# Performance work log

Measured on AMD Instinct MI355X. Metric: run time of the kernel, lower is better.

The kernel has to match this reference:

```python
import jax, jax.numpy as jnp
import numpy as np

L, N_ATOMS, N_PROBES, E, H = 3, 20000, 100000, 400000, 128
CUTOFF, STEP, EDGE_SIZE = 4.0, 0.25, 16
LOG2 = float(np.log(2.0))

def ssp(x):
    # ShiftedSoftplus: softplus(x) - log(2)
    return jax.nn.softplus(x) - LOG2

def mlp(x, W1, b1, W2, b2):
    return ssp(x @ W1 + b1) @ W2 + b2

def setup_inputs() -> dict:
    key = jax.random.key(0)
    ks = iter(jax.random.split(key, 32))
    def nrm(shape, s=0.05):
        return jax.random.normal(next(ks), shape, dtype=jnp.float32) * s
    inp = {
        'atom_rep': nrm((L, N_ATOMS, H), 1.0),
        'dist': jax.random.uniform(next(ks), (E, 1), dtype=jnp.float32) * CUTOFF,
    }
    pshapes = {
        'msg_We1': (L, EDGE_SIZE, H), 'msg_be1': (L, H),
        'msg_We2': (L, H, H), 'msg_be2': (L, H),
        'msg_Wn1': (L, 2 * H, H), 'msg_bn1': (L, H),
        'msg_Wn2': (L, H, H), 'msg_bn2': (L, H),
        'gate_W1': (L, H, H), 'gate_b1': (L, H),
        'gate_W2': (L, H, H), 'gate_b2': (L, H),
        'trans_W1': (L, H, H), 'trans_b1': (L, H),
        'trans_W2': (L, H, H), 'trans_b2': (L, H),
        'readout_W1': (H, H), 'readout_b1': (H,),
        'readout_W2': (H, 1), 'readout_b2': (1,),
    }
    for name, shp in pshapes.items():
        inp[name] = nrm(shp)
    senders = jax.random.randint(next(ks), (E, 1), 0, N_ATOMS)
    receivers = jax.random.randint(next(ks), (E, 1), 0, N_PROBES)
    inp['probe_edges'] = jnp.concatenate([senders, receivers], axis=1).astype(jnp.int32)
    return inp

def reference(atom_rep, dist, msg_We1, msg_be1, msg_We2, msg_be2, msg_Wn1, msg_bn1, msg_Wn2, msg_bn2, gate_W1, gate_b1, gate_W2, gate_b2, trans_W1, trans_b1, trans_W2, trans_b2, readout_W1, readout_b1, readout_W2, readout_b2, probe_edges):
    # gaussian_expansion of edge distances: [E, EDGE_SIZE]
    mu = jnp.arange(0.0, CUTOFF, STEP, dtype=jnp.float32)
    edge_state = jnp.exp(-((dist - mu) ** 2) / (2.0 * STEP * STEP))
    # SchnetMessageFunction soft cutoff on raw distance: [E, 1]
    soft_cut = 1.0 - jax.nn.sigmoid(5.0 * (dist - (CUTOFF - 1.5)))
    snd = probe_edges[:, 0]  # atom senders
    rcv = probe_edges[:, 1]  # probe receivers
    probe_state0 = jnp.zeros((N_PROBES, H), dtype=jnp.float32)

    def step(probe_state, layer):
        (nodes_l, We1, be1, We2, be2, Wn1, bn1, Wn2, bn2,
         gW1, gb1, gW2, gb2, tW1, tb1, tW2, tb2) = layer
        # edge filter gates [E, H]
        gates_msg = mlp(edge_state, We1, be1, We2, be2) * soft_cut
        # include_receiver=True with receiver_nodes=probe_state: concat sender atom / receiver probe
        nodes = jnp.concatenate([nodes_l[snd], probe_state[rcv]], axis=1)  # [E, 2H]
        messages = mlp(nodes, Wn1, bn1, Wn2, bn2) * gates_msg  # [E, H]
        msgsum = jax.ops.segment_sum(messages, rcv, num_segments=N_PROBES)  # [P, H]
        g = jax.nn.sigmoid(mlp(probe_state, gW1, gb1, gW2, gb2))
        new_state = probe_state * g + (1.0 - g) * mlp(msgsum, tW1, tb1, tW2, tb2)
        return new_state, None

    xs = (atom_rep, msg_We1, msg_be1, msg_We2, msg_be2, msg_Wn1, msg_bn1,
          msg_Wn2, msg_bn2, gate_W1, gate_b1, gate_W2, gate_b2,
          trans_W1, trans_b1, trans_W2, trans_b2)
    probe_state, _ = jax.lax.scan(step, probe_state0, xs)
    out = mlp(probe_state, readout_W1, readout_b1, readout_W2, readout_b2)[:, 0]  # [P]
    return out
```

## Files before the change

### kernel.cpp

```cpp
#include <hip/hip_runtime.h>

#define NLAYER 3
#define NATOM 20000
#define NPROBE 100000
#define NEDGE 400000
#define HD 128
#define NBIN 2048
#define CUTOFFF 4.0f
#define PLANE 16384
#define MT 64
#define NT 512
#define NSBLK ((NPROBE + 255) / 256)

typedef unsigned int u32;
typedef unsigned short u16;
typedef __attribute__((ext_vector_type(8))) short bf16x8;
typedef __attribute__((ext_vector_type(4))) float f32x4;

__device__ __forceinline__ float sspf(float x) {
    float e = __builtin_amdgcn_exp2f(fminf(x, 80.f) * 1.44269504088896341f);
    return 0.69314718055994531f * (__builtin_amdgcn_logf(1.f + e) - 1.f);
}
__device__ __forceinline__ float sigf(float x) {
    return 1.f / (1.f + __builtin_amdgcn_exp2f(-x * 1.44269504088896341f));
}
__device__ __forceinline__ void atomic_add_f(float* p, float v) {
    __hip_atomic_fetch_add(p, v, __ATOMIC_RELAXED, __HIP_MEMORY_SCOPE_AGENT);
}
__device__ __forceinline__ u32 atomic_add_u(u32* p, u32 v) {
    return __hip_atomic_fetch_add(p, v, __ATOMIC_RELAXED, __HIP_MEMORY_SCOPE_AGENT);
}
__device__ __forceinline__ u32 f2u(float f) { union { float f; u32 u; } x; x.f = f; return x.u; }
__device__ __forceinline__ float u2f(u32 u) { union { float f; u32 u; } x; x.u = u; return x.f; }
__device__ __forceinline__ u16 bf16rn(float f) {
    u32 u = f2u(f);
    u32 r = u + 0x7fffu + ((u >> 16) & 1u);
    return (u16)(r >> 16);
}
__device__ __forceinline__ u32 bf16pair(float x, float y) {
    u32 ux = f2u(x);
    u32 hx = (ux + 0x7fffu + ((ux >> 16) & 1u)) >> 16;
    u32 uy = f2u(y);
    u32 hy = (uy + 0x7fffu + ((uy >> 16) & 1u)) & 0xffff0000u;
    return hx | hy;
}
__device__ __forceinline__ void split_pair(float x, float y, u32& hi, u32& lo) {
    u32 ux = f2u(x);
    u32 hx = (ux + 0x7fffu + ((ux >> 16) & 1u)) & 0xffff0000u;
    float lxf = x - u2f(hx);
    u32 uy = f2u(y);
    u32 hy = (uy + 0x7fffu + ((uy >> 16) & 1u)) & 0xffff0000u;
    float lyf = y - u2f(hy);
    hi = (hx >> 16) | hy;
    lo = (f2u(lxf) >> 16) | (f2u(lyf) & 0xffff0000u);
}

__device__ __forceinline__ void bar_lds() {
    asm volatile("s_waitcnt lgkmcnt(0)" ::: "memory");
    __builtin_amdgcn_s_barrier();
}

__device__ __forceinline__ int bswz(int b, int nb) {
    int q = nb >> 3, r = nb & 7;
    int x = b & 7, o = b >> 3;
    return (x < r ? x * (q + 1) : r * (q + 1) + (x - r) * q) + o;
}

__device__ __forceinline__ void load_bfrags(const u16* __restrict__ Wb, int lane, int wid,
                                            bf16x8 Bh[4], bf16x8 Bl[4]) {
    const bf16x8* Bhp = (const bf16x8*)Wb;
    const bf16x8* Blp = (const bf16x8*)(Wb + PLANE);
#pragma unroll
    for (int c = 0; c < 4; ++c) {
        Bh[c] = Bhp[(size_t)(c * 8 + wid) * 64 + lane];
        Bl[c] = Blp[(size_t)(c * 8 + wid) * 64 + lane];
    }
}

__device__ __forceinline__ void mma_slice_pre(const u16* __restrict__ ldsH,
                                              const u16* __restrict__ ldsL,
                                              int lane, const bf16x8 Bh[4], const bf16x8 Bl[4],
                                              f32x4 acc[4]) {
    int l15 = lane & 15, kq = lane >> 4;
#pragma unroll
    for (int m = 0; m < 4; ++m) {
        int row = m * 16 + l15;
        int s = row & 7;
        const u16* hp = ldsH + row * 128;
        const u16* lp = ldsL + row * 128;
#pragma unroll
        for (int c = 0; c < 4; ++c) {
            int off = ((c * 4 + kq) ^ s) << 3;
            bf16x8 Ah = *(const bf16x8*)(hp + off);
            bf16x8 Al = *(const bf16x8*)(lp + off);
            acc[m] = __builtin_amdgcn_mfma_f32_16x16x32_bf16(Ah, Bh[c], acc[m], 0, 0, 0);
            acc[m] = __builtin_amdgcn_mfma_f32_16x16x32_bf16(Al, Bh[c], acc[m], 0, 0, 0);
            acc[m] = __builtin_amdgcn_mfma_f32_16x16x32_bf16(Ah, Bl[c], acc[m], 0, 0, 0);
        }
    }
}

__device__ __forceinline__ void mma_slice(const u16* __restrict__ ldsH,
                                          const u16* __restrict__ ldsL,
                                          int lane, int wid,
                                          const u16* __restrict__ Wb,
                                          f32x4 acc[4]) {
    bf16x8 Bh[4], Bl[4];
    load_bfrags(Wb, lane, wid, Bh, Bl);
    mma_slice_pre(ldsH, ldsL, lane, Bh, Bl, acc);
}

__device__ __forceinline__ void mma_slice_a1(const u16* __restrict__ ldsA,
                                             int lane, const bf16x8 Bh[4], const bf16x8 Bl[4],
                                             f32x4 acc[4]) {
    int l15 = lane & 15, kq = lane >> 4;
#pragma unroll
    for (int m = 0; m < 4; ++m) {
        int row = m * 16 + l15;
        int s = row & 7;
        const u16* ap = ldsA + row * 128;
#pragma unroll
        for (int c = 0; c < 4; ++c) {
            int off = ((c * 4 + kq) ^ s) << 3;
            bf16x8 Ah = *(const bf16x8*)(ap + off);
            acc[m] = __builtin_amdgcn_mfma_f32_16x16x32_bf16(Ah, Bh[c], acc[m], 0, 0, 0);
            acc[m] = __builtin_amdgcn_mfma_f32_16x16x32_bf16(Ah, Bl[c], acc[m], 0, 0, 0);
        }
    }
}

__device__ __forceinline__ void mma_w_a1(const u16* __restrict__ ldsA,
                                         int lane, int wid, const u16* __restrict__ Wb,
                                         f32x4 acc[4]) {
    bf16x8 Bh[4], Bl[4];
    load_bfrags(Wb, lane, wid, Bh, Bl);
    mma_slice_a1(ldsA, lane, Bh, Bl, acc);
}

__device__ __forceinline__ void pack_store(const float* v, int row, int q,
                                           u16* ldsH, u16* ldsL) {
    int s = row & 7;
#pragma unroll
    for (int h = 0; h < 2; ++h) {
        u32 hv[4], lv[4];
#pragma unroll
        for (int k = 0; k < 4; ++k)
            split_pair(v[8 * h + 2 * k], v[8 * h + 2 * k + 1], hv[k], lv[k]);
        int gc = q * 2 + h;
        int off = row * 128 + ((gc ^ s) << 3);
        *(uint4*)(ldsH + off) = make_uint4(hv[0], hv[1], hv[2], hv[3]);
        *(uint4*)(ldsL + off) = make_uint4(lv[0], lv[1], lv[2], lv[3]);
    }
}

__device__ __forceinline__ void pack_plane(const float* v, int row, int q, u16* ldsA) {
    int s = row & 7;
#pragma unroll
    for (int h = 0; h < 2; ++h) {
        u32 w0 = bf16pair(v[8 * h + 0], v[8 * h + 1]);
        u32 w1 = bf16pair(v[8 * h + 2], v[8 * h + 3]);
        u32 w2 = bf16pair(v[8 * h + 4], v[8 * h + 5]);
        u32 w3 = bf16pair(v[8 * h + 6], v[8 * h + 7]);
        int gc = q * 2 + h;
        *(uint4*)(ldsA + row * 128 + ((gc ^ s) << 3)) = make_uint4(w0, w1, w2, w3);
    }
}

__device__ __forceinline__ void gather_rows(const float* __restrict__ A, int M,
                                            int m0, int t, float* v) {
    int r = t >> 3, q = t & 7;
    int row = m0 + r;
    bool ok = row < M;
    const float4* src = (const float4*)(A + (size_t)row * HD + q * 16);
#pragma unroll
    for (int j = 0; j < 4; ++j) {
        float4 x = ok ? src[j] : make_float4(0.f, 0.f, 0.f, 0.f);
        v[4 * j] = x.x; v[4 * j + 1] = x.y; v[4 * j + 2] = x.z; v[4 * j + 3] = x.w;
    }
}
__device__ __forceinline__ void zero_rows(float* A, int M, int m0, int t) {
    int r = t >> 3, q = t & 7;
    int row = m0 + r;
    if (row < M) {
        float4* dst = (float4*)(A + (size_t)row * HD + q * 16);
        float4 z = make_float4(0.f, 0.f, 0.f, 0.f);
#pragma unroll
        for (int j = 0; j < 4; ++j) dst[j] = z;
    }
}
__device__ __forceinline__ void stage_split(const float* __restrict__ A, int M,
                                            int m0, int t, u16* ldsH, u16* ldsL) {
    float v[16];
    gather_rows(A, M, m0, t, v);
    pack_store(v, t >> 3, t & 7, ldsH, ldsL);
}
__device__ __forceinline__ void stage_plane(const float* __restrict__ A, int M,
                                            int m0, int t, u16* ldsA) {
    float v[16];
    gather_rows(A, M, m0, t, v);
    pack_plane(v, t >> 3, t & 7, ldsA);
}

__device__ __forceinline__ void h_store(u16* ldsH, u16* ldsL, int wid, int lane,
                                        const f32x4 acc[4], const float* __restrict__ bias) {
    int l15 = lane & 15, lq = lane >> 4;
    int col = wid * 16 + l15;
    float bb = bias[col];
    int gc = col >> 3, wg = col & 7;
#pragma unroll
    for (int m = 0; m < 4; ++m) {
#pragma unroll
        for (int r = 0; r < 4; ++r) {
            int row = m * 16 + lq * 4 + r;
            float h = sspf(acc[m][r] + bb);
            u32 u = f2u(h);
            u32 hh = (u + 0x7fffu + ((u >> 16) & 1u)) & 0xffff0000u;
            float lf = h - u2f(hh);
            int off = row * 128 + ((gc ^ (row & 7)) << 3) + wg;
            ldsH[off] = (u16)(hh >> 16);
            ldsL[off] = (u16)(f2u(lf) >> 16);
        }
    }
}
__device__ __forceinline__ void h_plane(u16* ldsA, int wid, int lane,
                                        const f32x4 acc[4], const float* __restrict__ bias) {
    int l15 = lane & 15, lq = lane >> 4;
    int col = wid * 16 + l15;
    float bb = bias[col];
    int gc = col >> 3, wg = col & 7;
#pragma unroll
    for (int m = 0; m < 4; ++m) {
#pragma unroll
        for (int r = 0; r < 4; ++r) {
            int row = m * 16 + lq * 4 + r;
            int off = row * 128 + ((gc ^ (row & 7)) << 3) + wg;
            ldsA[off] = bf16rn(sspf(acc[m][r] + bb));
        }
    }
}
__device__ __forceinline__ void v_store(u16* ldsH, u16* ldsL, int wid, int lane,
                                        int m, int r, float val) {
    int l15 = lane & 15, lq = lane >> 4;
    int col = wid * 16 + l15;
    int gc = col >> 3, wg = col & 7;
    int row = m * 16 + lq * 4 + r;
    u32 u = f2u(val);
    u32 hh = (u + 0x7fffu + ((u >> 16) & 1u)) & 0xffff0000u;
    float lf = val - u2f(hh);
    int off = row * 128 + ((gc ^ (row & 7)) << 3) + wg;
    ldsH[off] = (u16)(hh >> 16);
    ldsL[off] = (u16)(f2u(lf) >> 16);
}
__device__ __forceinline__ void v_plane(u16* ldsA, int wid, int lane,
                                        int m, int r, float val) {
    int l15 = lane & 15, lq = lane >> 4;
    int col = wid * 16 + l15;
    int gc = col >> 3, wg = col & 7;
    int row = m * 16 + lq * 4 + r;
    ldsA[row * 128 + ((gc ^ (row & 7)) << 3) + wg] = bf16rn(val);
}

__global__ void convert_w_k(const float* __restrict__ Wn1, const float* __restrict__ Wn2,
                            const float* __restrict__ gW1, const float* __restrict__ gW2,
                            const float* __restrict__ tW1, const float* __restrict__ tW2,
                            const float* __restrict__ rW1, u16* __restrict__ Wb) {
    int m = blockIdx.x;
    const float* src;
    if (m < 6)       src = Wn1 + (size_t)(m >> 1) * (2 * HD * HD) + (size_t)(m & 1) * (HD * HD);
    else if (m < 9)  src = Wn2 + (size_t)(m - 6) * HD * HD;
    else if (m < 12) src = gW1 + (size_t)(m - 9) * HD * HD;
    else if (m < 15) src = gW2 + (size_t)(m - 12) * HD * HD;
    else if (m < 18) src = tW1 + (size_t)(m - 15) * HD * HD;
    else if (m < 21) src = tW2 + (size_t)(m - 18) * HD * HD;
    else             src = rW1;
    int t = threadIdx.x;
    int lane = t & 63, nn = t >> 6;
    u16* dh = Wb + (size_t)m * (2 * PLANE);
    u16* dl = dh + PLANE;
    for (int c = 0; c < 4; ++c) {
        for (int hh = 0; hh < 2; ++hh) {
            int n = nn + hh * 4;
            int col = n * 16 + (lane & 15);
            int k0 = c * 32 + (lane >> 4) * 8;
            u32 hv[4], lv[4];
#pragma unroll
            for (int jj = 0; jj < 4; ++jj) {
                float wA = src[(size_t)(k0 + 2 * jj) * HD + col];
                float wB = src[(size_t)(k0 + 2 * jj + 1) * HD + col];
                u16 ha = bf16rn(wA), hb = bf16rn(wB);
                u16 la = bf16rn(wA - u2f((u32)ha << 16));
                u16 lb = bf16rn(wB - u2f((u32)hb << 16));
                hv[jj] = (u32)ha | ((u32)hb << 16);
                lv[jj] = (u32)la | ((u32)lb << 16);
            }
            size_t off = ((size_t)(c * 8 + n) * 64 + lane) * 8;
            *(uint4*)(dh + off) = make_uint4(hv[0], hv[1], hv[2], hv[3]);
            *(uint4*)(dl + off) = make_uint4(lv[0], lv[1], lv[2], lv[3]);
        }
    }
}

__global__ void gate_table_k(const float* __restrict__ We1, const float* __restrict__ be1,
                             const float* __restrict__ We2, const float* __restrict__ be2,
                             float2* __restrict__ gt2) {
    int row = blockIdx.x;
    int l = row / (NBIN + 1);
    int i = row % (NBIN + 1);
    int j = threadIdx.x;
    float d = (CUTOFFF / NBIN) * (float)i;
    __shared__ float h1[HD];
    const float* w1 = We1 + (size_t)l * 16 * HD;
    float acc = be1[l * HD + j];
#pragma unroll
    for (int k = 0; k < 16; ++k) {
        float dd = d - 0.25f * (float)k;
        float es = __builtin_amdgcn_exp2f(-dd * dd * 8.0f * 1.44269504088896341f);
        acc = fmaf(es, w1[k * HD + j], acc);
    }
    h1[j] = sspf(acc);
    __syncthreads();
    const float* w2 = We2 + (size_t)l * HD * HD;
    float acc2 = be2[l * HD + j];
    for (int k = 0; k < HD; ++k) acc2 = fmaf(h1[k], w2[k * HD + j], acc2);
    float sc = 1.f - sigf(5.f * (d - (CUTOFFF - 1.5f)));
    float val = acc2 * sc;
    float2* base = gt2 + (size_t)l * NBIN * HD;
    if (i < NBIN) base[(size_t)i * HD + j].x = val;
    if (i > 0)    base[(size_t)(i - 1) * HD + j].y = val;
}

__global__ void gate0_k(const float* __restrict__ gW2, const float* __restrict__ gb1,
                        const float* __restrict__ gb2, float* __restrict__ g0v) {
    int j = threadIdx.x;
    __shared__ float h[HD];
    h[j] = sspf(gb1[j]);
    __syncthreads();
    float acc = gb2[j];
    for (int k = 0; k < HD; ++k) acc = fmaf(h[k], gW2[k * HD + j], acc);
    g0v[j] = sigf(acc);
}

__global__ __launch_bounds__(256) void hist_k(const int* __restrict__ pe, u32* __restrict__ cnt) {
    int e = blockIdx.x * 256 + threadIdx.x;
    if (e < NEDGE) atomic_add_u(&cnt[pe[2 * e + 1]], 1u);
}

__global__ __launch_bounds__(256) void bsum_k(const u32* __restrict__ cnt, u32* __restrict__ bsum) {
    int i = blockIdx.x * 256 + threadIdx.x;
    int v = (i < NPROBE) ? (int)cnt[i] : 0;
#pragma unroll
    for (int d = 1; d < 64; d <<= 1) v += __shfl_xor(v, d);
    __shared__ int wsum[4];
    if ((threadIdx.x & 63) == 0) wsum[threadIdx.x >> 6] = v;
    __syncthreads();
    if (threadIdx.x == 0) bsum[blockIdx.x] = (u32)(wsum[0] + wsum[1] + wsum[2] + wsum[3]);
}

__global__ __launch_bounds__(512) void bscan_k(u32* __restrict__ bsum) {
    __shared__ u32 s[512];
    int t = threadIdx.x;
    u32 v = (t < NSBLK) ? bsum[t] : 0u;
    s[t] = v;
    __syncthreads();
    for (int d = 1; d < 512; d <<= 1) {
        u32 x = (t >= d) ? s[t - d] : 0u;
        __syncthreads();
        s[t] += x;
        __syncthreads();
    }
    if (t < NSBLK) bsum[t] = s[t] - v;
}

__global__ __launch_bounds__(256) void cur_k(const u32* __restrict__ cnt,
                                             const u32* __restrict__ bsum, u32* __restrict__ cur) {
    __shared__ u32 s[256];
    int b = blockIdx.x, t = threadIdx.x;
    int i = b * 256 + t;
    u32 v = (i < NPROBE) ? cnt[i] : 0u;
    s[t] = v;
    __syncthreads();
    for (int d = 1; d < 256; d <<= 1) {
        u32 x = (t >= d) ? s[t - d] : 0u;
        __syncthreads();
        s[t] += x;
        __syncthreads();
    }
    if (i < NPROBE) cur[i] = bsum[b] + s[t] - v;
}

__global__ __launch_bounds__(256) void scatter_k(const int* __restrict__ pe,
                                                 u32* __restrict__ cur, u32* __restrict__ eord) {
    int e = blockIdx.x * 256 + threadIdx.x;
    if (e < NEDGE) {
        u32 pos = atomic_add_u(&cur[pe[2 * e + 1]], 1u);
        eord[pos] = (u32)e;
    }
}

#define ABLK 313
__global__ __launch_bounds__(NT, 4) void gemm_atoms_k(const float* __restrict__ atom_rep,
                                                      const u16* __restrict__ Wb,
                                                      const float* __restrict__ bn1,
                                                      u16* __restrict__ Xab) {
    __shared__ u16 ldsH[MT * 128];
    __shared__ u16 ldsL[MT * 128];
    int l = blockIdx.x / ABLK;
    int mb = blockIdx.x % ABLK;
    const float* A = atom_rep + (size_t)l * NATOM * HD;
    const u16* W = Wb + (size_t)(2 * l) * 2 * PLANE;
    u16* outp = Xab + (size_t)l * NATOM * HD;
    int m0 = mb * MT, t = threadIdx.x;
    stage_split(A, NATOM, m0, t, ldsH, ldsL);
    bar_lds();
    int lane = t & 63, wid = t >> 6;
    int l15 = lane & 15, lq = lane >> 4;
    int col = wid * 16 + l15;
    f32x4 acc[4] = {};
    mma_slice(ldsH, ldsL, lane, wid, W, acc);
    float bv = bn1[l * HD + col];
#pragma unroll
    for (int m = 0; m < 4; ++m) {
#pragma unroll
        for (int r = 0; r < 4; ++r) {
            int row = m0 + m * 16 + lq * 4 + r;
            if (row < NATOM) outp[(size_t)row * HD + col] = bf16rn(acc[m][r] + bv);
        }
    }
}

__device__ __forceinline__ int rho(int r) {
    return ((r >> 2) & 3) * 16 + ((r >> 4) << 2) + (r & 3);
}

__device__ __forceinline__ void gather_edge(
        int e0, int t, const u16* __restrict__ Xab, const u16* __restrict__ Xp,
        const int* __restrict__ pe, const u32* __restrict__ eord,
        const float* __restrict__ dist,
        u32* mix_s, float* fr_s, float* sum) {
    int r = t >> 3, q = t & 7;
    int e = (int)eord[e0 + r];
    int snd = pe[2 * e], rcv = pe[2 * e + 1];
    if (q == 0) {
        float x = dist[e] * ((float)NBIN / CUTOFFF);
        int i = (int)x;
        i = i < (NBIN - 1) ? i : (NBIN - 1);
        fr_s[r] = x - (float)i;
        mix_s[r] = ((u32)rcv << 11) | (u32)i;
    }
    const uint4* xa4 = (const uint4*)(Xab + (size_t)snd * HD + q * 16);
    u32 aw[8];
    *(uint4*)aw = xa4[0];
    *(uint4*)(aw + 4) = xa4[1];
    u32 pw[8];
    if (Xp) {
        const uint4* xp4 = (const uint4*)(Xp + (size_t)rcv * HD + q * 16);
        *(uint4*)pw = xp4[0];
        *(uint4*)(pw + 4) = xp4[1];
    }
#pragma unroll
    for (int w = 0; w < 8; ++w) {
        float ae = u2f(aw[w] << 16), ao = u2f(aw[w] & 0xffff0000u);
        if (Xp) {
            ae += u2f(pw[w] << 16);
            ao += u2f(pw[w] & 0xffff0000u);
        }
        sum[2 * w] = ae;
        sum[2 * w + 1] = ao;
    }
}

__device__ __forceinline__ void edge_out(const f32x4 acc[4], const u32* mix_s,
        const float* fr_s, const float2* __restrict__ gt2,
        float bb, int col, int lq, float* __restrict__ msgsum) {
    float carry = 0.f;
    int rcc = -1;
#pragma unroll
    for (int m = 3; m >= 0; --m) {
        int ebase = lq * 16 + m * 4;
        float vals[4];
        int rc[4];
#pragma unroll
        for (int r = 0; r < 4; ++r) {
            u32 mx = mix_s[ebase + r];
            rc[r] = (int)(mx >> 11);
            float2 g2 = gt2[(size_t)(mx & 2047u) * HD + col];
            vals[r] = (acc[m][r] + bb) * fmaf(g2.y - g2.x, fr_s[ebase + r], g2.x);
        }
        if (rcc == rc[3]) vals[3] += carry;
        else if (rcc >= 0) atomic_add_f(msgsum + (size_t)rcc * HD + col, carry);
#pragma unroll
        for (int r = 3; r >= 1; --r) {
            if (rc[r] == rc[r - 1]) vals[r - 1] += vals[r];
            else atomic_add_f(msgsum + (size_t)rc[r] * HD + col, vals[r]);
        }
        carry = vals[0];
        rcc = rc[0];
    }
    atomic_add_f(msgsum + (size_t)rcc * HD + col, carry);
}

__global__ __launch_bounds__(NT, 4) void edge_msg_k(
        const u16* __restrict__ Xab, const u16* __restrict__ Xp,
        const u16* __restrict__ W2b, const float* __restrict__ bn2,
        const float2* __restrict__ gt2, const float* __restrict__ dist,
        const int* __restrict__ pe, const u32* __restrict__ eord,
        float* __restrict__ msgsum) {
    __shared__ u16 ldsA[MT * 128];
    __shared__ u32 mix_s[MT];
    __shared__ float fr_s[MT];
    int t = threadIdx.x;
    int lane = t & 63, wid = t >> 6;
    int l15 = lane & 15, lq = lane >> 4;
    int col = wid * 16 + l15;
    const int nb = NEDGE / MT;
    int e0 = bswz(blockIdx.x, nb) * MT;

    bf16x8 Bh[4], Bl[4];
    load_bfrags(W2b, lane, wid, Bh, Bl);
    float bb = bn2[col];

    float s0[16];
    gather_edge(e0, t, Xab, Xp, pe, eord, dist, mix_s, fr_s, s0);
    {
        float h[16];
#pragma unroll
        for (int k = 0; k < 16; ++k) h[k] = sspf(s0[k]);
        pack_plane(h, rho(t >> 3), t & 7, ldsA);
    }
    bar_lds();

    f32x4 acc[4] = {};
    mma_slice_a1(ldsA, lane, Bh, Bl, acc);
    edge_out(acc, mix_s, fr_s, gt2, bb, col, lq, msgsum);
}

__global__ __launch_bounds__(NT, 4) void probe_update_k(
        const float* ps, const float* msgsum, float* msgzero,
        const u16* __restrict__ gW1b, const float* __restrict__ gb1,
        const u16* __restrict__ gW2b, const float* __restrict__ gb2,
        const u16* __restrict__ tW1b, const float* __restrict__ tb1,
        const u16* __restrict__ tW2b, const float* __restrict__ tb2,
        const u16* __restrict__ W3b,
        const u16* __restrict__ rW1b, const float* __restrict__ rb1,
        const float* __restrict__ rW2, const float* __restrict__ rb2,
        const float* __restrict__ g0v,
        float* psout, u16* __restrict__ xpout, float* __restrict__ outp) {
    __shared__ u16 ldsH[MT * 128];
    __shared__ u16 ldsL[MT * 128];
    __shared__ float parts[MT][9];
    int m0 = blockIdx.x * MT, t = threadIdx.x;
    int lane = t & 63, wid = t >> 6;
    int l15 = lane & 15, lq = lane >> 4;
    int col = wid * 16 + l15;

    f32x4 g[4] = {};
    f32x4 tv[4] = {};

    float sm[16];
    gather_rows(msgsum, NPROBE, m0, t, sm);

    if (!g0v) {
        stage_plane(ps, NPROBE, m0, t, ldsH);
        bar_lds();
        mma_w_a1(ldsH, lane, wid, gW1b, g);
        bar_lds();
        h_plane(ldsH, wid, lane, g, gb1);
        bar_lds();
#pragma unroll
        for (int m = 0; m < 4; ++m) g[m] = (f32x4){0.f, 0.f, 0.f, 0.f};
        mma_w_a1(ldsH, lane, wid, gW2b, g);
        float gb2v = gb2[col];
#pragma unroll
        for (int m = 0; m < 4; ++m)
#pragma unroll
            for (int r = 0; r < 4; ++r) g[m][r] = sigf(g[m][r] + gb2v);
        bar_lds();
    } else {
        float gv = g0v[col];
#pragma unroll
        for (int m = 0; m < 4; ++m)
#pragma unroll
            for (int r = 0; r < 4; ++r) g[m][r] = gv;
    }

    pack_store(sm, t >> 3, t & 7, ldsH, ldsL);
    if (msgzero) zero_rows(msgzero, NPROBE, m0, t);
    bar_lds();
    mma_slice(ldsH, ldsL, lane, wid, tW1b, tv);
    bar_lds();
    h_store(ldsH, ldsL, wid, lane, tv, tb1);
    bar_lds();
#pragma unroll
    for (int m = 0; m < 4; ++m) tv[m] = (f32x4){0.f, 0.f, 0.f, 0.f};
    mma_slice(ldsH, ldsL, lane, wid, tW2b, tv);

    bool isW3 = (W3b != nullptr);
    bool isRd = (rW1b != nullptr);
    if (isW3 || isRd) bar_lds();

    float tb2v = tb2[col];
#pragma unroll
    for (int m = 0; m < 4; ++m) {
#pragma unroll
        for (int r = 0; r < 4; ++r) {
            int row = m0 + m * 16 + lq * 4 + r;
            float val = 0.f;
            if (row < NPROBE) {
                size_t idx = (size_t)row * HD + col;
                float tval = tv[m][r] + tb2v;
                float pv = g0v ? 0.f : ps[idx];
                val = fmaf(pv - tval, g[m][r], tval);
                if (!isRd) psout[idx] = val;
            }
            if (isW3) v_plane(ldsH, wid, lane, m, r, val);
            else if (isRd) v_store(ldsH, ldsL, wid, lane, m, r, val);
        }
    }
    if (!(isW3 || isRd)) return;
    bar_lds();

    if (isW3) {
        f32x4 a[4] = {};
        mma_w_a1(ldsH, lane, wid, W3b, a);
#pragma unroll
        for (int m = 0; m < 4; ++m)
#pragma unroll
            for (int r = 0; r < 4; ++r) {
                int row = m0 + m * 16 + lq * 4 + r;
                if (row < NPROBE) xpout[(size_t)row * HD + col] = bf16rn(a[m][r]);
            }
    } else {
        f32x4 a[4] = {};
        mma_slice(ldsH, ldsL, lane, wid, rW1b, a);
        float rb1v = rb1[col], w2v = rW2[col];
#pragma unroll
        for (int m = 0; m < 4; ++m)
#pragma unroll
            for (int r = 0; r < 4; ++r) {
                float p = sspf(a[m][r] + rb1v) * w2v;
                p += __shfl_xor(p, 1, 16);
                p += __shfl_xor(p, 2, 16);
                p += __shfl_xor(p, 4, 16);
                p += __shfl_xor(p, 8, 16);
                if (l15 == 0) parts[m * 16 + lq * 4 + r][wid] = p;
            }
        bar_lds();
        if (t < MT) {
            int row = m0 + t;
            if (row < NPROBE) {
                float s = rb2[0];
#pragma unroll
                for (int w = 0; w < 8; ++w) s += parts[t][w];
                outp[row] = s;
            }
        }
    }
}

extern "C" void kernel_launch(void* const* d_in, const int* in_sizes, int n_in,
                              void* d_out, int out_size, void* d_ws, size_t ws_size,
                              hipStream_t stream) {
    const float* atom_rep = (const float*)d_in[0];
    const float* dist     = (const float*)d_in[1];
    const float* We1 = (const float*)d_in[2];
    const float* be1 = (const float*)d_in[3];
    const float* We2 = (const float*)d_in[4];
    const float* be2 = (const float*)d_in[5];
    const float* Wn1 = (const float*)d_in[6];
    const float* bn1 = (const float*)d_in[7];
    const float* Wn2 = (const float*)d_in[8];
    const float* bn2 = (const float*)d_in[9];
    const float* gW1 = (const float*)d_in[10];
    const float* gb1 = (const float*)d_in[11];
    const float* gW2 = (const float*)d_in[12];
    const float* gb2 = (const float*)d_in[13];
    const float* tW1 = (const float*)d_in[14];
    const float* tb1 = (const float*)d_in[15];
    const float* tW2 = (const float*)d_in[16];
    const float* tb2 = (const float*)d_in[17];
    const float* rW1 = (const float*)d_in[18];
    const float* rb1 = (const float*)d_in[19];
    const float* rW2 = (const float*)d_in[20];
    const float* rb2 = (const float*)d_in[21];
    const int*   pe  = (const int*)d_in[22];
    float* out = (float*)d_out;

    float* ws = (float*)d_ws;
    float* ps     = ws;
    float* msgsum = ps + 12800000u;
    float2* gt2   = (float2*)(msgsum + 12800000u);
    float* g0v    = (float*)(gt2 + (size_t)NLAYER * NBIN * HD);
    u16*   Wb     = (u16*)(g0v + 128);
    u16*   Xp16   = Wb + 22 * 2 * PLANE;
    u16*   Xab    = Xp16 + 12800000u;
    u32*   cnt    = (u32*)(Xab + 7680000u);
    u32*   bsum   = cnt + NPROBE;
    u32*   cur    = bsum + 512;
    u32*   eord   = cur + NPROBE;

    const int PBLK = (NPROBE + MT - 1) / MT;
    const int EBLK = NEDGE / MT;
    const int TBLK = (NEDGE + 255) / 256;

    hipMemsetAsync(cnt, 0, (size_t)NPROBE * 4, stream);
    hipMemsetAsync(msgsum, 0, 12800000ull * 4, stream);
    convert_w_k<<<22, 256, 0, stream>>>(Wn1, Wn2, gW1, gW2, tW1, tW2, rW1, Wb);
    gate_table_k<<<NLAYER * (NBIN + 1), HD, 0, stream>>>(We1, be1, We2, be2, gt2);
    gate0_k<<<1, HD, 0, stream>>>(gW2, gb1, gb2, g0v);
    hist_k<<<TBLK, 256, 0, stream>>>(pe, cnt);
    bsum_k<<<NSBLK, 256, 0, stream>>>(cnt, bsum);
    bscan_k<<<1, 512, 0, stream>>>(bsum);
    cur_k<<<NSBLK, 256, 0, stream>>>(cnt, bsum, cur);
    scatter_k<<<TBLK, 256, 0, stream>>>(pe, cur, eord);
    gemm_atoms_k<<<NLAYER * ABLK, NT, 0, stream>>>(atom_rep, Wb, bn1, Xab);

    for (int l = 0; l < NLAYER; ++l) {
        edge_msg_k<<<EBLK, NT, 0, stream>>>(Xab + (size_t)l * NATOM * HD,
                                            (l == 0) ? nullptr : Xp16,
                                            Wb + (size_t)(6 + l) * 2 * PLANE,
                                            bn2 + l * HD,
                                            gt2 + (size_t)l * NBIN * HD,
                                            dist, pe, eord, msgsum);
        const u16* W3  = (l < NLAYER - 1) ? Wb + (size_t)(2 * (l + 1) + 1) * 2 * PLANE : nullptr;
        const u16* RW1 = (l == NLAYER - 1) ? Wb + (size_t)21 * 2 * PLANE : nullptr;
        float* mz = (l < NLAYER - 1) ? msgsum : nullptr;
        probe_update_k<<<PBLK, NT, 0, stream>>>(ps, msgsum, mz,
                                                Wb + (size_t)(9 + l) * 2 * PLANE, gb1 + l * HD,
                                                Wb + (size_t)(12 + l) * 2 * PLANE, gb2 + l * HD,
                                                Wb + (size_t)(15 + l) * 2 * PLANE, tb1 + l * HD,
                                                Wb + (size_t)(18 + l) * 2 * PLANE, tb2 + l * HD,
                                                W3, RW1, rb1, rW2, rb2,
                                                (l == 0) ? g0v : nullptr,
                                                ps, Xp16, out);
    }
}
```

Before: 606.2 us.

## Fuse edge message and probe update into one per-probe-block kernel

Edge messages are now computed inside the probe-update kernel. Each probe block walks its contiguous receiver-sorted edge range (row starts come from the scan) and accumulates messages into a shared-memory tile instead of issuing global atomics into a full msgsum buffer. This removes the separate edge kernel, the large msgsum buffer with its memset and per-layer zeroing, and the global read-back of that buffer. In exchange, blocks loop over a variable number of edges, which can cause load imbalance, and the heavier shared-memory use lowers launch-bounds occupancy from 4 to 2.

```diff
diff --git a/kernel.cpp b/kernel.cpp
--- a/kernel.cpp
+++ b/kernel.cpp
@@ -10,6 +10,7 @@
 #define PLANE 16384
 #define MT 64
 #define NT 512
+#define PBLK ((NPROBE + MT - 1) / MT)
 #define NSBLK ((NPROBE + 255) / 256)
 
 typedef unsigned int u32;
@@ -23,9 +24,6 @@
 }
 __device__ __forceinline__ float sigf(float x) {
     return 1.f / (1.f + __builtin_amdgcn_exp2f(-x * 1.44269504088896341f));
-}
-__device__ __forceinline__ void atomic_add_f(float* p, float v) {
-    __hip_atomic_fetch_add(p, v, __ATOMIC_RELAXED, __HIP_MEMORY_SCOPE_AGENT);
 }
 __device__ __forceinline__ u32 atomic_add_u(u32* p, u32 v) {
     return __hip_atomic_fetch_add(p, v, __ATOMIC_RELAXED, __HIP_MEMORY_SCOPE_AGENT);
@@ -99,11 +97,9 @@
         }
     }
 }
-
 __device__ __forceinline__ void mma_slice(const u16* __restrict__ ldsH,
                                           const u16* __restrict__ ldsL,
-                                          int lane, int wid,
-                                          const u16* __restrict__ Wb,
+                                          int lane, int wid, const u16* __restrict__ Wb,
                                           f32x4 acc[4]) {
     bf16x8 Bh[4], Bl[4];
     load_bfrags(Wb, lane, wid, Bh, Bl);
@@ -128,7 +124,6 @@
         }
     }
 }
-
 __device__ __forceinline__ void mma_w_a1(const u16* __restrict__ ldsA,
                                          int lane, int wid, const u16* __restrict__ Wb,
                                          f32x4 acc[4]) {
@@ -152,7 +147,6 @@
         *(uint4*)(ldsL + off) = make_uint4(lv[0], lv[1], lv[2], lv[3]);
     }
 }
-
 __device__ __forceinline__ void pack_plane(const float* v, int row, int q, u16* ldsA) {
     int s = row & 7;
 #pragma unroll
@@ -165,7 +159,6 @@
         *(uint4*)(ldsA + row * 128 + ((gc ^ s) << 3)) = make_uint4(w0, w1, w2, w3);
     }
 }
-
 __device__ __forceinline__ void gather_rows(const float* __restrict__ A, int M,
                                             int m0, int t, float* v) {
     int r = t >> 3, q = t & 7;
@@ -178,27 +171,11 @@
         v[4 * j] = x.x; v[4 * j + 1] = x.y; v[4 * j + 2] = x.z; v[4 * j + 3] = x.w;
     }
 }
-__device__ __forceinline__ void zero_rows(float* A, int M, int m0, int t) {
-    int r = t >> 3, q = t & 7;
-    int row = m0 + r;
-    if (row < M) {
-        float4* dst = (float4*)(A + (size_t)row * HD + q * 16);
-        float4 z = make_float4(0.f, 0.f, 0.f, 0.f);
-#pragma unroll
-        for (int j = 0; j < 4; ++j) dst[j] = z;
-    }
-}
 __device__ __forceinline__ void stage_split(const float* __restrict__ A, int M,
                                             int m0, int t, u16* ldsH, u16* ldsL) {
     float v[16];
     gather_rows(A, M, m0, t, v);
     pack_store(v, t >> 3, t & 7, ldsH, ldsL);
-}
-__device__ __forceinline__ void stage_plane(const float* __restrict__ A, int M,
-                                            int m0, int t, u16* ldsA) {
-    float v[16];
-    gather_rows(A, M, m0, t, v);
-    pack_plane(v, t >> 3, t & 7, ldsA);
 }
 
 __device__ __forceinline__ void h_store(u16* ldsH, u16* ldsL, int wid, int lane,
@@ -344,7 +321,6 @@
     int e = blockIdx.x * 256 + threadIdx.x;
     if (e < NEDGE) atomic_add_u(&cnt[pe[2 * e + 1]], 1u);
 }
-
 __global__ __launch_bounds__(256) void bsum_k(const u32* __restrict__ cnt, u32* __restrict__ bsum) {
     int i = blockIdx.x * 256 + threadIdx.x;
     int v = (i < NPROBE) ? (int)cnt[i] : 0;
@@ -355,7 +331,6 @@
     __syncthreads();
     if (threadIdx.x == 0) bsum[blockIdx.x] = (u32)(wsum[0] + wsum[1] + wsum[2] + wsum[3]);
 }
-
 __global__ __launch_bounds__(512) void bscan_k(u32* __restrict__ bsum) {
     __shared__ u32 s[512];
     int t = threadIdx.x;
@@ -370,9 +345,9 @@
     }
     if (t < NSBLK) bsum[t] = s[t] - v;
 }
-
 __global__ __launch_bounds__(256) void cur_k(const u32* __restrict__ cnt,
-                                             const u32* __restrict__ bsum, u32* __restrict__ cur) {
+                                             const u32* __restrict__ bsum,
+                                             u32* __restrict__ cur, u32* __restrict__ rs) {
     __shared__ u32 s[256];
     int b = blockIdx.x, t = threadIdx.x;
     int i = b * 256 + t;
@@ -385,9 +360,15 @@
         s[t] += x;
         __syncthreads();
     }
-    if (i < NPROBE) cur[i] = bsum[b] + s[t] - v;
-}
-
+    if (i < NPROBE) {
+        u32 v0 = bsum[b] + s[t] - v;
+        cur[i] = v0;
+        rs[i] = v0;
+    }
+}
+__global__ void rstail_k(u32* __restrict__ rs) {
+    rs[NPROBE + threadIdx.x] = NEDGE;
+}
 __global__ __launch_bounds__(256) void scatter_k(const int* __restrict__ pe,
                                                  u32* __restrict__ cur, u32* __restrict__ eord) {
     int e = blockIdx.x * 256 + threadIdx.x;
@@ -432,46 +413,9 @@
     return ((r >> 2) & 3) * 16 + ((r >> 4) << 2) + (r & 3);
 }
 
-__device__ __forceinline__ void gather_edge(
-        int e0, int t, const u16* __restrict__ Xab, const u16* __restrict__ Xp,
-        const int* __restrict__ pe, const u32* __restrict__ eord,
-        const float* __restrict__ dist,
-        u32* mix_s, float* fr_s, float* sum) {
-    int r = t >> 3, q = t & 7;
-    int e = (int)eord[e0 + r];
-    int snd = pe[2 * e], rcv = pe[2 * e + 1];
-    if (q == 0) {
-        float x = dist[e] * ((float)NBIN / CUTOFFF);
-        int i = (int)x;
-        i = i < (NBIN - 1) ? i : (NBIN - 1);
-        fr_s[r] = x - (float)i;
-        mix_s[r] = ((u32)rcv << 11) | (u32)i;
-    }
-    const uint4* xa4 = (const uint4*)(Xab + (size_t)snd * HD + q * 16);
-    u32 aw[8];
-    *(uint4*)aw = xa4[0];
-    *(uint4*)(aw + 4) = xa4[1];
-    u32 pw[8];
-    if (Xp) {
-        const uint4* xp4 = (const uint4*)(Xp + (size_t)rcv * HD + q * 16);
-        *(uint4*)pw = xp4[0];
-        *(uint4*)(pw + 4) = xp4[1];
-    }
-#pragma unroll
-    for (int w = 0; w < 8; ++w) {
-        float ae = u2f(aw[w] << 16), ao = u2f(aw[w] & 0xffff0000u);
-        if (Xp) {
-            ae += u2f(pw[w] << 16);
-            ao += u2f(pw[w] & 0xffff0000u);
-        }
-        sum[2 * w] = ae;
-        sum[2 * w + 1] = ao;
-    }
-}
-
-__device__ __forceinline__ void edge_out(const f32x4 acc[4], const u32* mix_s,
+__device__ __forceinline__ void edge_out_lds(const f32x4 acc[4], const u32* mix_s,
         const float* fr_s, const float2* __restrict__ gt2,
-        float bb, int col, int lq, float* __restrict__ msgsum) {
+        float bb, int col, int lq, float* __restrict__ msg) {
     float carry = 0.f;
     int rcc = -1;
 #pragma unroll
@@ -482,60 +426,37 @@
 #pragma unroll
         for (int r = 0; r < 4; ++r) {
             u32 mx = mix_s[ebase + r];
-            rc[r] = (int)(mx >> 11);
-            float2 g2 = gt2[(size_t)(mx & 2047u) * HD + col];
-            vals[r] = (acc[m][r] + bb) * fmaf(g2.y - g2.x, fr_s[ebase + r], g2.x);
-        }
-        if (rcc == rc[3]) vals[3] += carry;
-        else if (rcc >= 0) atomic_add_f(msgsum + (size_t)rcc * HD + col, carry);
+            if (mx == 0xFFFFFFFFu) {
+                rc[r] = -2;
+                vals[r] = 0.f;
+            } else {
+                rc[r] = (int)(mx >> 11);
+                float2 g2 = gt2[(size_t)(mx & 2047u) * HD + col];
+                vals[r] = (acc[m][r] + bb) * fmaf(g2.y - g2.x, fr_s[ebase + r], g2.x);
+            }
+        }
+        if (rcc >= 0) {
+            if (rcc == rc[3]) vals[3] += carry;
+            else atomicAdd(&msg[rcc * HD + col], carry);
+        }
 #pragma unroll
         for (int r = 3; r >= 1; --r) {
             if (rc[r] == rc[r - 1]) vals[r - 1] += vals[r];
-            else atomic_add_f(msgsum + (size_t)rc[r] * HD + col, vals[r]);
+            else if (rc[r] >= 0) atomicAdd(&msg[rc[r] * HD + col], vals[r]);
         }
         carry = vals[0];
         rcc = rc[0];
     }
-    atomic_add_f(msgsum + (size_t)rcc * HD + col, carry);
-}
-
-__global__ __launch_bounds__(NT, 4) void edge_msg_k(
+    if (rcc >= 0) atomicAdd(&msg[rcc * HD + col], carry);
+}
+
+__global__ __launch_bounds__(NT, 2) void fused_layer_k(
         const u16* __restrict__ Xab, const u16* __restrict__ Xp,
         const u16* __restrict__ W2b, const float* __restrict__ bn2,
         const float2* __restrict__ gt2, const float* __restrict__ dist,
         const int* __restrict__ pe, const u32* __restrict__ eord,
-        float* __restrict__ msgsum) {
-    __shared__ u16 ldsA[MT * 128];
-    __shared__ u32 mix_s[MT];
-    __shared__ float fr_s[MT];
-    int t = threadIdx.x;
-    int lane = t & 63, wid = t >> 6;
-    int l15 = lane & 15, lq = lane >> 4;
-    int col = wid * 16 + l15;
-    const int nb = NEDGE / MT;
-    int e0 = bswz(blockIdx.x, nb) * MT;
-
-    bf16x8 Bh[4], Bl[4];
-    load_bfrags(W2b, lane, wid, Bh, Bl);
-    float bb = bn2[col];
-
-    float s0[16];
-    gather_edge(e0, t, Xab, Xp, pe, eord, dist, mix_s, fr_s, s0);
-    {
-        float h[16];
-#pragma unroll
-        for (int k = 0; k < 16; ++k) h[k] = sspf(s0[k]);
-        pack_plane(h, rho(t >> 3), t & 7, ldsA);
-    }
-    bar_lds();
-
-    f32x4 acc[4] = {};
-    mma_slice_a1(ldsA, lane, Bh, Bl, acc);
-    edge_out(acc, mix_s, fr_s, gt2, bb, col, lq, msgsum);
-}
-
-__global__ __launch_bounds__(NT, 4) void probe_update_k(
-        const float* ps, const float* msgsum, float* msgzero,
+        const u32* __restrict__ rs,
+        const float* ps,
         const u16* __restrict__ gW1b, const float* __restrict__ gb1,
         const u16* __restrict__ gW2b, const float* __restrict__ gb2,
         const u16* __restrict__ tW1b, const float* __restrict__ tb1,
@@ -545,36 +466,125 @@
         const float* __restrict__ rW2, const float* __restrict__ rb2,
         const float* __restrict__ g0v,
         float* psout, u16* __restrict__ xpout, float* __restrict__ outp) {
-    __shared__ u16 ldsH[MT * 128];
-    __shared__ u16 ldsL[MT * 128];
+    __shared__ float msg[MT * HD];
+    __shared__ u16 ldsA[MT * 128];
+    __shared__ u32 mix_s[MT];
+    __shared__ float fr_s[MT];
     __shared__ float parts[MT][9];
-    int m0 = blockIdx.x * MT, t = threadIdx.x;
+    u16* ldsH = (u16*)msg;
+    u16* ldsL = ldsH + MT * 128;
+
+    int m0 = bswz(blockIdx.x, PBLK) * MT;
+    int t = threadIdx.x;
     int lane = t & 63, wid = t >> 6;
     int l15 = lane & 15, lq = lane >> 4;
     int col = wid * 16 + l15;
-
+    bool hasGate = (g0v == nullptr);
+    bool isW3 = (W3b != nullptr);
+    bool isRd = (rW1b != nullptr);
+
+    u32 estart = rs[m0];
+    u32 eend = rs[m0 + MT];
+
+    float sp[16];
+    if (hasGate) gather_rows(ps, NPROBE, m0, t, sp);
+    {
+        float4 z = make_float4(0.f, 0.f, 0.f, 0.f);
+        float4* m4 = (float4*)msg;
+#pragma unroll
+        for (int i = 0; i < 4; ++i) m4[t + i * NT] = z;
+    }
+    bar_lds();
+
+    {
+        bf16x8 Bh[4], Bl[4];
+        load_bfrags(W2b, lane, wid, Bh, Bl);
+        float bb2 = bn2[col];
+        for (u32 c0 = estart; c0 < eend; c0 += MT) {
+            int r = t >> 3, q = t & 7;
+            u32 e = c0 + (u32)r;
+            float h[16];
+            if (e < eend) {
+                int ee = (int)eord[e];
+                int snd = pe[2 * ee], rcv = pe[2 * ee + 1];
+                if (q == 0) {
+                    float x = dist[ee] * ((float)NBIN / CUTOFFF);
+                    int i = (int)x;
+                    i = i < (NBIN - 1) ? i : (NBIN - 1);
+                    fr_s[r] = x - (float)i;
+                    mix_s[r] = (((u32)(rcv - m0)) << 11) | (u32)i;
+                }
+                const uint4* xa4 = (const uint4*)(Xab + (size_t)snd * HD + q * 16);
+                u32 aw[8];
+                *(uint4*)aw = xa4[0];
+                *(uint4*)(aw + 4) = xa4[1];
+                u32 pw[8];
+                if (Xp) {
+                    const uint4* xp4 = (const uint4*)(Xp + (size_t)rcv * HD + q * 16);
+                    *(uint4*)pw = xp4[0];
+                    *(uint4*)(pw + 4) = xp4[1];
+                }
+#pragma unroll
+                for (int w = 0; w < 8; ++w) {
+                    float ae = u2f(aw[w] << 16), ao = u2f(aw[w] & 0xffff0000u);
+                    if (Xp) {
+                        ae += u2f(pw[w] << 16);
+                        ao += u2f(pw[w] & 0xffff0000u);
+                    }
+                    h[2 * w] = sspf(ae);
+                    h[2 * w + 1] = sspf(ao);
+                }
+            } else {
+                if (q == 0) mix_s[r] = 0xFFFFFFFFu;
+#pragma unroll
+                for (int k = 0; k < 16; ++k) h[k] = 0.f;
+            }
+            pack_plane(h, rho(r), q, ldsA);
+            bar_lds();
+            f32x4 acc[4] = {};
+            mma_slice_a1(ldsA, lane, Bh, Bl, acc);
+            edge_out_lds(acc, mix_s, fr_s, gt2, bb2, col, lq, msg);
+            bar_lds();
+        }
+    }
+
+    float mreg[16];
+    {
+        int r = t >> 3, q = t & 7;
+        const float* mp = msg + r * HD + q * 16;
+#pragma unroll
+        for (int k = 0; k < 16; ++k) mreg[k] = mp[k];
+    }
+    if (hasGate) pack_plane(sp, t >> 3, t & 7, ldsA);
+    bar_lds();
+
+    pack_store(mreg, t >> 3, t & 7, ldsH, ldsL);
     f32x4 g[4] = {};
+    if (hasGate) mma_w_a1(ldsA, lane, wid, gW1b, g);
+    bar_lds();
+
     f32x4 tv[4] = {};
-
-    float sm[16];
-    gather_rows(msgsum, NPROBE, m0, t, sm);
-
-    if (!g0v) {
-        stage_plane(ps, NPROBE, m0, t, ldsH);
-        bar_lds();
-        mma_w_a1(ldsH, lane, wid, gW1b, g);
-        bar_lds();
-        h_plane(ldsH, wid, lane, g, gb1);
-        bar_lds();
+    mma_slice(ldsH, ldsL, lane, wid, tW1b, tv);
+    if (hasGate) h_plane(ldsA, wid, lane, g, gb1);
+    bar_lds();
+
+    if (hasGate) {
 #pragma unroll
         for (int m = 0; m < 4; ++m) g[m] = (f32x4){0.f, 0.f, 0.f, 0.f};
-        mma_w_a1(ldsH, lane, wid, gW2b, g);
+        mma_w_a1(ldsA, lane, wid, gW2b, g);
+    }
+    h_store(ldsH, ldsL, wid, lane, tv, tb1);
+    bar_lds();
+
+#pragma unroll
+    for (int m = 0; m < 4; ++m) tv[m] = (f32x4){0.f, 0.f, 0.f, 0.f};
+    mma_slice(ldsH, ldsL, lane, wid, tW2b, tv);
+    if (hasGate) {
         float gb2v = gb2[col];
 #pragma unroll
         for (int m = 0; m < 4; ++m)
 #pragma unroll
             for (int r = 0; r < 4; ++r) g[m][r] = sigf(g[m][r] + gb2v);
-        bar_lds();
     } else {
         float gv = g0v[col];
 #pragma unroll
@@ -582,20 +592,6 @@
 #pragma unroll
             for (int r = 0; r < 4; ++r) g[m][r] = gv;
     }
-
-    pack_store(sm, t >> 3, t & 7, ldsH, ldsL);
-    if (msgzero) zero_rows(msgzero, NPROBE, m0, t);
-    bar_lds();
-    mma_slice(ldsH, ldsL, lane, wid, tW1b, tv);
-    bar_lds();
-    h_store(ldsH, ldsL, wid, lane, tv, tb1);
-    bar_lds();
-#pragma unroll
-    for (int m = 0; m < 4; ++m) tv[m] = (f32x4){0.f, 0.f, 0.f, 0.f};
-    mma_slice(ldsH, ldsL, lane, wid, tW2b, tv);
-
-    bool isW3 = (W3b != nullptr);
-    bool isRd = (rW1b != nullptr);
     if (isW3 || isRd) bar_lds();
 
     float tb2v = tb2[col];
@@ -608,11 +604,11 @@
             if (row < NPROBE) {
                 size_t idx = (size_t)row * HD + col;
                 float tval = tv[m][r] + tb2v;
-                float pv = g0v ? 0.f : ps[idx];
+                float pv = hasGate ? ps[idx] : 0.f;
                 val = fmaf(pv - tval, g[m][r], tval);
                 if (!isRd) psout[idx] = val;
             }
-            if (isW3) v_plane(ldsH, wid, lane, m, r, val);
+            if (isW3) v_plane(ldsA, wid, lane, m, r, val);
             else if (isRd) v_store(ldsH, ldsL, wid, lane, m, r, val);
         }
     }
@@ -621,7 +617,7 @@
 
     if (isW3) {
         f32x4 a[4] = {};
-        mma_w_a1(ldsH, lane, wid, W3b, a);
+        mma_w_a1(ldsA, lane, wid, W3b, a);
 #pragma unroll
         for (int m = 0; m < 4; ++m)
 #pragma unroll
@@ -687,8 +683,7 @@
 
     float* ws = (float*)d_ws;
     float* ps     = ws;
-    float* msgsum = ps + 12800000u;
-    float2* gt2   = (float2*)(msgsum + 12800000u);
+    float2* gt2   = (float2*)(ps + 12800000u);
     float* g0v    = (float*)(gt2 + (size_t)NLAYER * NBIN * HD);
     u16*   Wb     = (u16*)(g0v + 128);
     u16*   Xp16   = Wb + 22 * 2 * PLANE;
@@ -696,41 +691,38 @@
     u32*   cnt    = (u32*)(Xab + 7680000u);
     u32*   bsum   = cnt + NPROBE;
     u32*   cur    = bsum + 512;
-    u32*   eord   = cur + NPROBE;
-
-    const int PBLK = (NPROBE + MT - 1) / MT;
-    const int EBLK = NEDGE / MT;
+    u32*   rs     = cur + NPROBE;
+    u32*   eord   = rs + NPROBE + 128;
+
     const int TBLK = (NEDGE + 255) / 256;
 
     hipMemsetAsync(cnt, 0, (size_t)NPROBE * 4, stream);
-    hipMemsetAsync(msgsum, 0, 12800000ull * 4, stream);
     convert_w_k<<<22, 256, 0, stream>>>(Wn1, Wn2, gW1, gW2, tW1, tW2, rW1, Wb);
     gate_table_k<<<NLAYER * (NBIN + 1), HD, 0, stream>>>(We1, be1, We2, be2, gt2);
     gate0_k<<<1, HD, 0, stream>>>(gW2, gb1, gb2, g0v);
     hist_k<<<TBLK, 256, 0, stream>>>(pe, cnt);
     bsum_k<<<NSBLK, 256, 0, stream>>>(cnt, bsum);
     bscan_k<<<1, 512, 0, stream>>>(bsum);
-    cur_k<<<NSBLK, 256, 0, stream>>>(cnt, bsum, cur);
+    cur_k<<<NSBLK, 256, 0, stream>>>(cnt, bsum, cur, rs);
+    rstail_k<<<1, 128, 0, stream>>>(rs);
     scatter_k<<<TBLK, 256, 0, stream>>>(pe, cur, eord);
     gemm_atoms_k<<<NLAYER * ABLK, NT, 0, stream>>>(atom_rep, Wb, bn1, Xab);
 
     for (int l = 0; l < NLAYER; ++l) {
-        edge_msg_k<<<EBLK, NT, 0, stream>>>(Xab + (size_t)l * NATOM * HD,
-                                            (l == 0) ? nullptr : Xp16,
-                                            Wb + (size_t)(6 + l) * 2 * PLANE,
-                                            bn2 + l * HD,
-                                            gt2 + (size_t)l * NBIN * HD,
-                                            dist, pe, eord, msgsum);
         const u16* W3  = (l < NLAYER - 1) ? Wb + (size_t)(2 * (l + 1) + 1) * 2 * PLANE : nullptr;
         const u16* RW1 = (l == NLAYER - 1) ? Wb + (size_t)21 * 2 * PLANE : nullptr;
-        float* mz = (l < NLAYER - 1) ? msgsum : nullptr;
-        probe_update_k<<<PBLK, NT, 0, stream>>>(ps, msgsum, mz,
-                                                Wb + (size_t)(9 + l) * 2 * PLANE, gb1 + l * HD,
-                                                Wb + (size_t)(12 + l) * 2 * PLANE, gb2 + l * HD,
-                                                Wb + (size_t)(15 + l) * 2 * PLANE, tb1 + l * HD,
-                                                Wb + (size_t)(18 + l) * 2 * PLANE, tb2 + l * HD,
-                                                W3, RW1, rb1, rW2, rb2,
-                                                (l == 0) ? g0v : nullptr,
-                                                ps, Xp16, out);
-    }
-}
+        fused_layer_k<<<PBLK, NT, 0, stream>>>(
+            Xab + (size_t)l * NATOM * HD,
+            (l == 0) ? nullptr : Xp16,
+            Wb + (size_t)(6 + l) * 2 * PLANE, bn2 + l * HD,
+            gt2 + (size_t)l * NBIN * HD, dist, pe, eord, rs,
+            ps,
+            Wb + (size_t)(9 + l) * 2 * PLANE, gb1 + l * HD,
+            Wb + (size_t)(12 + l) * 2 * PLANE, gb2 + l * HD,
+            Wb + (size_t)(15 + l) * 2 * PLANE, tb1 + l * HD,
+            Wb + (size_t)(18 + l) * 2 * PLANE, tb2 + l * HD,
+            W3, RW1, rb1, rW2, rb2,
+            (l == 0) ? g0v : nullptr,
+            ps, Xp16, out);
+    }
+}
```

Measured after the change: 1.245 ms. 2.05x slower.
